# Kernel tuning notes

Measured on AMD Instinct MI355X. Metric: run time of the kernel, lower is better.

Reference implementation:

```python
import jax, jax.numpy as jnp
import numpy as np

TOP_K = 2
NUM_EXPERTS = 8


def setup_inputs() -> dict:
    key = jax.random.key(0)
    ks = jax.random.split(key, 9)
    B, S, N, H = 1, 8, 1024, 512
    E, I_moe, I_sh = NUM_EXPERTS, 2048 // TOP_K, 2048
    s = 0.02
    return {
        "hidden_states": jax.random.normal(ks[0], (B, S, N, H), dtype=jnp.float32),
        "gate_w": jax.random.normal(ks[1], (E, H), dtype=jnp.float32) * s,
        "expert_w1": jax.random.normal(ks[2], (E, I_moe, H), dtype=jnp.float32) * s,
        "expert_w2": jax.random.normal(ks[3], (E, H, I_moe), dtype=jnp.float32) * s,
        "expert_w3": jax.random.normal(ks[4], (E, I_moe, H), dtype=jnp.float32) * s,
        "shared_w1": jax.random.normal(ks[5], (I_sh, H), dtype=jnp.float32) * s,
        "shared_w2": jax.random.normal(ks[6], (H, I_sh), dtype=jnp.float32) * s,
        "shared_w3": jax.random.normal(ks[7], (I_sh, H), dtype=jnp.float32) * s,
        "shared_gate_w": jax.random.normal(ks[8], (1, H), dtype=jnp.float32) * s,
    }


def reference(hidden_states, gate_w, expert_w1, expert_w2, expert_w3,
              shared_w1, shared_w2, shared_w3, shared_gate_w):
    B, S, N, H = hidden_states.shape
    x = hidden_states.reshape(-1, H)                       # [T, H], T = B*S*N

    # Router: softmax in fp32, then top-k (norm_topk_prob=False).
    router_logits = x @ gate_w.T                           # [T, E]
    probs = jax.nn.softmax(router_logits.astype(jnp.float32), axis=-1)
    top_w, top_i = jax.lax.top_k(probs, TOP_K)             # [T, k]
    # Combine weight per (token, expert): zero for unselected experts.
    combine = jnp.sum(top_w[..., None] * jax.nn.one_hot(top_i, NUM_EXPERTS, dtype=probs.dtype), axis=1)
    combine = combine.astype(x.dtype)                      # [T, E]

    # Routed experts (SwiGLU FFN per expert), evaluated densely and masked
    # by the sparse combine weights (same math as gather/scatter dispatch).
    h1 = jnp.einsum('th,eih->tei', x, expert_w1)           # [T, E, I_moe]
    h3 = jnp.einsum('th,eih->tei', x, expert_w3)
    h = jax.nn.silu(h1) * h3
    expert_out = jnp.einsum('tei,ehi->teh', h, expert_w2)  # [T, E, H]
    moe_out = jnp.einsum('te,teh->th', combine, expert_out)

    # Shared expert with sigmoid gate.
    sh = (jax.nn.silu(x @ shared_w1.T) * (x @ shared_w3.T)) @ shared_w2.T
    sgate = jax.nn.sigmoid(x @ shared_gate_w.T)            # [T, 1]
    out = moe_out + sgate * sh

    return out.reshape(B, S, N, H), router_logits
```

## Files before the change

### kernel.cpp

```cpp
#include <hip/hip_runtime.h>
#include <hip/hip_bf16.h>
#include <stdint.h>
#include <math.h>

typedef __bf16 bf16;
typedef bf16 bf16x8 __attribute__((ext_vector_type(8)));
typedef bf16 bf16x4 __attribute__((ext_vector_type(4)));
typedef float f32x4 __attribute__((ext_vector_type(4)));
typedef unsigned int u32;

#define TOKENS 8192
#define HD 512
#define NE 8
#define IM 1024
#define ISH 2048
#define CAP 2560

__device__ __forceinline__ void gld16(const void* g, void* l) {
  __builtin_amdgcn_global_load_lds(
      (const __attribute__((address_space(1))) u32*)g,
      (__attribute__((address_space(3))) u32*)l, 16, 0, 0);
}

#define RT_BLOCKS (TOKENS / 4)
#define CVT_BLOCKS 3840
#define CVT_STRIDE (CVT_BLOCKS * 256)
#define F4_E  (NE * IM * HD / 4)
#define F4_S  (ISH * HD / 4)
#define F4_C1 (F4_E)
#define F4_C2 (F4_C1 + F4_E)
#define F4_C3 (F4_C2 + F4_S)
#define F4_C4 (F4_C3 + F4_S)
#define F4_C5 (F4_C4 + F4_E)
#define F4_TOT (F4_C5 + F4_S)

__launch_bounds__(256)
__global__ void router_cvt_k(const float* __restrict__ x, const float* __restrict__ gw,
                             const float* __restrict__ sgw, float* __restrict__ logits,
                             float* __restrict__ sgate, int* __restrict__ topi,
                             float* __restrict__ topw, int* __restrict__ counts,
                             bf16* __restrict__ xb,
                             const float* __restrict__ e1, const float* __restrict__ e3,
                             const float* __restrict__ s1, const float* __restrict__ s3,
                             const float* __restrict__ e2, const float* __restrict__ s2,
                             bf16* __restrict__ wdst) {
  if (blockIdx.x >= RT_BLOCKS) {
    int idx = (blockIdx.x - RT_BLOCKS) * 256 + threadIdx.x;
#pragma unroll
    for (int it = 0; it < 4; it++, idx += CVT_STRIDE) {
      const float* s; int off;
      if (idx < F4_C1)      { s = e1; off = idx; }
      else if (idx < F4_C2) { s = e3; off = idx - F4_C1; }
      else if (idx < F4_C3) { s = s1; off = idx - F4_C2; }
      else if (idx < F4_C4) { s = s3; off = idx - F4_C3; }
      else if (idx < F4_C5) { s = e2; off = idx - F4_C4; }
      else                  { s = s2; off = idx - F4_C5; }
      const float4 v = ((const float4*)s)[off];
      bf16x4 o;
      o.x = (bf16)v.x; o.y = (bf16)v.y; o.z = (bf16)v.z; o.w = (bf16)v.w;
      ((bf16x4*)wdst)[idx] = o;
    }
    return;
  }
  if (blockIdx.x == 0 && threadIdx.x < NE) counts[threadIdx.x] = 0;
  __shared__ float gws[9][512];
  for (int i = threadIdx.x; i < 9 * 512; i += 256) {
    int r = i >> 9, c = i & 511;
    float v = (r < 8) ? gw[i] : sgw[c];
    gws[r][((c & 7) << 6) | (c >> 3)] = v;
  }
  __syncthreads();
  int wave = threadIdx.x >> 6, lane = threadIdx.x & 63;
  int t = blockIdx.x * 4 + wave;
  const float* xp = x + (size_t)t * HD + lane * 8;
  float4 va = *(const float4*)xp;
  float4 vb = *(const float4*)(xp + 4);
  float xv[8] = {va.x, va.y, va.z, va.w, vb.x, vb.y, vb.z, vb.w};
  {
    bf16x8 xo;
#pragma unroll
    for (int j = 0; j < 8; j++) xo[j] = (bf16)xv[j];
    *(bf16x8*)(xb + (size_t)t * HD + lane * 8) = xo;
  }
  float acc[9];
#pragma unroll
  for (int e = 0; e < 9; e++) {
    float a = 0.f;
#pragma unroll
    for (int j = 0; j < 8; j++) a = fmaf(xv[j], gws[e][j * 64 + lane], a);
    acc[e] = a;
  }
#pragma unroll
  for (int off = 32; off > 0; off >>= 1) {
#pragma unroll
    for (int e = 0; e < 9; e++) acc[e] += __shfl_down(acc[e], off);
  }
  if (lane == 0) {
    float mx = acc[0];
#pragma unroll
    for (int e = 1; e < 8; e++) mx = fmaxf(mx, acc[e]);
    float p[8], sum = 0.f;
#pragma unroll
    for (int e = 0; e < 8; e++) { p[e] = expf(acc[e] - mx); sum += p[e]; }
    float inv = 1.f / sum;
    int i0 = 0; float b0 = p[0];
#pragma unroll
    for (int e = 1; e < 8; e++) if (p[e] > b0) { b0 = p[e]; i0 = e; }
    int i1 = -1; float b1 = -1.f;
#pragma unroll
    for (int e = 0; e < 8; e++) if (e != i0 && p[e] > b1) { b1 = p[e]; i1 = e; }
#pragma unroll
    for (int e = 0; e < 8; e++) logits[(size_t)t * 8 + e] = acc[e];
    topi[2 * t] = i0; topi[2 * t + 1] = i1;
    topw[2 * t] = b0 * inv; topw[2 * t + 1] = b1 * inv;
    sgate[t] = 1.f / (1.f + expf(-acc[8]));
  }
}

__launch_bounds__(256)
__global__ void dispatch_k(const int* __restrict__ topi, const float* __restrict__ topw,
                           int* __restrict__ counts, int* __restrict__ tok,
                           float* __restrict__ wl, int* __restrict__ pos) {
  __shared__ int lcnt[NE];
  __shared__ int lbase[NE];
  int tid = threadIdx.x;
  if (tid < NE) lcnt[tid] = 0;
  __syncthreads();
  int t = blockIdx.x * 256 + tid;
  int e0 = topi[2 * t], e1 = topi[2 * t + 1];
  float w0 = topw[2 * t], w1 = topw[2 * t + 1];
  int r0 = atomicAdd(&lcnt[e0], 1);
  int r1 = atomicAdd(&lcnt[e1], 1);
  __syncthreads();
  if (tid < NE) lbase[tid] = atomicAdd(&counts[tid], lcnt[tid]);
  __syncthreads();
  int p0 = lbase[e0] + r0;
  int p1 = lbase[e1] + r1;
  if (p0 < CAP) { tok[e0 * CAP + p0] = t; wl[e0 * CAP + p0] = w0; }
  if (p1 < CAP) { tok[e1 * CAP + p1] = t; wl[e1 * CAP + p1] = w1; }
  pos[2 * t]     = (p0 < CAP) ? e0 * CAP + p0 : -1;
  pos[2 * t + 1] = (p1 < CAP) ? e1 * CAP + p1 : -1;
}

__launch_bounds__(256, 4)
__global__ void gemm1_k(const bf16* __restrict__ X, const int* __restrict__ tokl,
                        const int* __restrict__ counts,
                        const bf16* __restrict__ e1w, const bf16* __restrict__ e3w,
                        const bf16* __restrict__ s1w, const bf16* __restrict__ s3w,
                        bf16* __restrict__ hmoe, bf16* __restrict__ hsh) {
  const bf16 *W1, *W3;
  bf16* Hout;
  const int* tl = nullptr;
  int cnt = 0, m0, n0, N;
  bool gather;
  int y = blockIdx.y;
  if (y < 160) {
    int e = y / 20, mt = y % 20;
    cnt = min(counts[e], CAP);
    if (mt * 128 >= cnt) return;
    gather = true;
    tl = tokl + e * CAP;
    W1 = e1w + (size_t)e * IM * HD;
    W3 = e3w + (size_t)e * IM * HD;
    Hout = hmoe + (size_t)e * CAP * IM;
    N = IM; m0 = mt * 128; n0 = blockIdx.x * 64;
  } else {
    int s = y - 160;
    gather = false;
    W1 = s1w; W3 = s3w; Hout = hsh; N = ISH;
    m0 = (s >> 1) * 128;
    n0 = ((s & 1) * 16 + blockIdx.x) * 64;
  }

  __shared__ __align__(16) bf16 As[2][128 * 32];
  __shared__ __align__(16) bf16 B1s[2][64 * 32];
  __shared__ __align__(16) bf16 B3s[2][64 * 32];

  int tid = threadIdx.x;
  int sr = tid >> 2;
  int colb = (tid & 3) * 16;
  int ar0, ar1;
  if (gather) {
    ar0 = tl[min(m0 + sr, cnt - 1)];
    ar1 = tl[min(m0 + 64 + sr, cnt - 1)];
  } else { ar0 = m0 + sr; ar1 = m0 + 64 + sr; }
  const char* apa = (const char*)(X + (size_t)ar0 * HD) + colb;
  const char* apb = (const char*)(X + (size_t)ar1 * HD) + colb;
  const char* bp1 = (const char*)(W1 + (size_t)(n0 + sr) * HD) + colb;
  const char* bp3 = (const char*)(W3 + (size_t)(n0 + sr) * HD) + colb;
  char* lA0a = (char*)&As[0][0] + tid * 16;
  char* lA0b = (char*)&As[1][0] + tid * 16;
  char* lA1a = (char*)&As[0][0] + 4096 + tid * 16;
  char* lA1b = (char*)&As[1][0] + 4096 + tid * 16;
  char* lB1a = (char*)&B1s[0][0] + tid * 16;
  char* lB1b = (char*)&B1s[1][0] + tid * 16;
  char* lB3a = (char*)&B3s[0][0] + tid * 16;
  char* lB3b = (char*)&B3s[1][0] + tid * 16;

  int wid = tid >> 6, lane = tid & 63;
  int wm = (wid >> 1) * 64, wn = (wid & 1) * 32;
  int lrow = lane & 15, lq = lane >> 4;

  f32x4 acc1[4][2] = {};
  f32x4 acc3[4][2] = {};

  for (int kb = 0; kb < 1024; kb += 128) {
    __syncthreads();
    gld16(apa + kb, lA0a);      gld16(apa + kb + 64, lA0b);
    gld16(apb + kb, lA1a);      gld16(apb + kb + 64, lA1b);
    gld16(bp1 + kb, lB1a);      gld16(bp1 + kb + 64, lB1b);
    gld16(bp3 + kb, lB3a);      gld16(bp3 + kb + 64, lB3b);
    __syncthreads();
#pragma unroll
    for (int ks = 0; ks < 2; ks++) {
      bf16x8 a[4], b1[2], b3[2];
#pragma unroll
      for (int i = 0; i < 4; i++)
        a[i] = *(const bf16x8*)&As[ks][(wm + i * 16 + lrow) * 32 + lq * 8];
#pragma unroll
      for (int j = 0; j < 2; j++) {
        b1[j] = *(const bf16x8*)&B1s[ks][(wn + j * 16 + lrow) * 32 + lq * 8];
        b3[j] = *(const bf16x8*)&B3s[ks][(wn + j * 16 + lrow) * 32 + lq * 8];
      }
#pragma unroll
      for (int i = 0; i < 4; i++)
#pragma unroll
        for (int j = 0; j < 2; j++) {
          acc1[i][j] = __builtin_amdgcn_mfma_f32_16x16x32_bf16(a[i], b1[j], acc1[i][j], 0, 0, 0);
          acc3[i][j] = __builtin_amdgcn_mfma_f32_16x16x32_bf16(a[i], b3[j], acc3[i][j], 0, 0, 0);
        }
    }
  }

#pragma unroll
  for (int i = 0; i < 4; i++)
#pragma unroll
    for (int r = 0; r < 4; r++) {
      int row = m0 + wm + i * 16 + lq * 4 + r;
#pragma unroll
      for (int j = 0; j < 2; j++) {
        float v1 = acc1[i][j][r], v3 = acc3[i][j][r];
        float hv = v1 / (1.f + __expf(-v1)) * v3;
        Hout[(size_t)row * N + (n0 + wn + j * 16 + lrow)] = (bf16)hv;
      }
    }
}

__launch_bounds__(256, 4)
__global__ void gemm2_k(const bf16* __restrict__ hmoe, const bf16* __restrict__ hsh,
                        const bf16* __restrict__ e2w, const bf16* __restrict__ s2w,
                        const float* __restrict__ wll, const int* __restrict__ counts,
                        bf16* __restrict__ yslot, bf16* __restrict__ ysh) {
  const bf16 *Hin, *W2;
  const float* wlp = nullptr;
  bf16* Yout;
  int cnt = 0, m0, K;
  bool weighted;
  int y = blockIdx.y;
  if (y < 64) {
    weighted = false;
    Hin = hsh; W2 = s2w; Yout = ysh; K = ISH; m0 = y * 128;
  } else {
    int e = (y - 64) / 20, mt = (y - 64) % 20;
    cnt = min(counts[e], CAP);
    if (mt * 128 >= cnt) return;
    weighted = true;
    Hin = hmoe + (size_t)e * CAP * IM;
    W2 = e2w + (size_t)e * HD * IM;
    wlp = wll + e * CAP;
    Yout = yslot + (size_t)e * CAP * HD;
    K = IM; m0 = mt * 128;
  }
  int n0 = blockIdx.x * 128;

  __shared__ __align__(16) bf16 As[2][128 * 32];
  __shared__ __align__(16) bf16 Bs[2][128 * 32];

  int tid = threadIdx.x;
  int sr = tid >> 2;
  int colb = (tid & 3) * 16;
  const char* apa = (const char*)(Hin + (size_t)(m0 + sr) * K) + colb;
  const char* apb = (const char*)(Hin + (size_t)(m0 + 64 + sr) * K) + colb;
  const char* bpa = (const char*)(W2 + (size_t)(n0 + sr) * K) + colb;
  const char* bpb = (const char*)(W2 + (size_t)(n0 + 64 + sr) * K) + colb;
  char* lA0a = (char*)&As[0][0] + tid * 16;
  char* lA0b = (char*)&As[1][0] + tid * 16;
  char* lA1a = (char*)&As[0][0] + 4096 + tid * 16;
  char* lA1b = (char*)&As[1][0] + 4096 + tid * 16;
  char* lB0a = (char*)&Bs[0][0] + tid * 16;
  char* lB0b = (char*)&Bs[1][0] + tid * 16;
  char* lB1a = (char*)&Bs[0][0] + 4096 + tid * 16;
  char* lB1b = (char*)&Bs[1][0] + 4096 + tid * 16;

  int wid = tid >> 6, lane = tid & 63;
  int wm = (wid >> 1) * 64, wn = (wid & 1) * 64;
  int lrow = lane & 15, lq = lane >> 4;

  f32x4 acc[4][4] = {};

  for (int kb = 0; kb < K * 2; kb += 128) {
    __syncthreads();
    gld16(apa + kb, lA0a);      gld16(apa + kb + 64, lA0b);
    gld16(apb + kb, lA1a);      gld16(apb + kb + 64, lA1b);
    gld16(bpa + kb, lB0a);      gld16(bpa + kb + 64, lB0b);
    gld16(bpb + kb, lB1a);      gld16(bpb + kb + 64, lB1b);
    __syncthreads();
#pragma unroll
    for (int ks = 0; ks < 2; ks++) {
      bf16x8 a[4], b[4];
#pragma unroll
      for (int i = 0; i < 4; i++) {
        a[i] = *(const bf16x8*)&As[ks][(wm + i * 16 + lrow) * 32 + lq * 8];
        b[i] = *(const bf16x8*)&Bs[ks][(wn + i * 16 + lrow) * 32 + lq * 8];
      }
#pragma unroll
      for (int i = 0; i < 4; i++)
#pragma unroll
        for (int j = 0; j < 4; j++)
          acc[i][j] = __builtin_amdgcn_mfma_f32_16x16x32_bf16(a[i], b[j], acc[i][j], 0, 0, 0);
    }
  }

#pragma unroll
  for (int i = 0; i < 4; i++)
#pragma unroll
    for (int r = 0; r < 4; r++) {
      int row = m0 + wm + i * 16 + lq * 4 + r;
      float w = weighted ? ((row < cnt) ? wlp[row] : 0.f) : 1.f;
      bf16* op = Yout + (size_t)row * HD;
#pragma unroll
      for (int j = 0; j < 4; j++)
        op[n0 + wn + j * 16 + lrow] = (bf16)(w * acc[i][j][r]);
    }
}

__launch_bounds__(256)
__global__ void combine_k(const bf16* __restrict__ yslot, const bf16* __restrict__ ysh,
                          const int* __restrict__ pos, const float* __restrict__ sgate,
                          float* __restrict__ out) {
  int wave = threadIdx.x >> 6, lane = threadIdx.x & 63;
  int t = blockIdx.x * 4 + wave;
  int p0 = pos[2 * t], p1 = pos[2 * t + 1];
  float g = sgate[t];
  int col = lane * 8;
  float acc[8];
  {
    const bf16x8 s = *(const bf16x8*)(ysh + (size_t)t * HD + col);
#pragma unroll
    for (int i = 0; i < 8; i++) acc[i] = g * (float)s[i];
  }
  if (p0 >= 0) {
    const bf16x8 v = *(const bf16x8*)(yslot + (size_t)p0 * HD + col);
#pragma unroll
    for (int i = 0; i < 8; i++) acc[i] += (float)v[i];
  }
  if (p1 >= 0) {
    const bf16x8 v = *(const bf16x8*)(yslot + (size_t)p1 * HD + col);
#pragma unroll
    for (int i = 0; i < 8; i++) acc[i] += (float)v[i];
  }
  float* op = out + (size_t)t * HD + col;
#pragma unroll
  for (int i = 0; i < 8; i++) op[i] = acc[i];
}

extern "C" void kernel_launch(void* const* d_in, const int* in_sizes, int n_in,
                              void* d_out, int out_size, void* d_ws, size_t ws_size,
                              hipStream_t stream) {
  const float* x   = (const float*)d_in[0];
  const float* gw  = (const float*)d_in[1];
  const float* ew1 = (const float*)d_in[2];
  const float* ew2 = (const float*)d_in[3];
  const float* ew3 = (const float*)d_in[4];
  const float* sw1 = (const float*)d_in[5];
  const float* sw2 = (const float*)d_in[6];
  const float* sw3 = (const float*)d_in[7];
  const float* sgw = (const float*)d_in[8];
  float* out = (float*)d_out;
  float* logits = out + (size_t)TOKENS * HD;

  char* w = (char*)d_ws;
  bf16* xb  = (bf16*)w; w += (size_t)TOKENS * HD * 2;
  bf16* e1b = (bf16*)w; w += (size_t)NE * IM * HD * 2;
  bf16* e3b = (bf16*)w; w += (size_t)NE * IM * HD * 2;
  bf16* s1b = (bf16*)w; w += (size_t)ISH * HD * 2;
  bf16* s3b = (bf16*)w; w += (size_t)ISH * HD * 2;
  bf16* e2b = (bf16*)w; w += (size_t)NE * HD * IM * 2;
  bf16* s2b = (bf16*)w; w += (size_t)HD * ISH * 2;
  float* sgate = (float*)w; w += TOKENS * 4;
  int*   topi  = (int*)w;   w += TOKENS * 2 * 4;
  float* topw  = (float*)w; w += TOKENS * 2 * 4;
  int*   counts = (int*)w;  w += 256;
  int*   tok   = (int*)w;   w += NE * CAP * 4;
  float* wl    = (float*)w; w += NE * CAP * 4;
  int*   pos   = (int*)w;   w += TOKENS * 2 * 4;
  bf16* hmoe = (bf16*)w; w += (size_t)NE * CAP * IM * 2;
  bf16* hsh  = (bf16*)w; w += (size_t)TOKENS * ISH * 2;
  bf16* yslot = xb;
  bf16* ysh   = (bf16*)((char*)xb + (size_t)NE * CAP * HD * 2);

  hipLaunchKernelGGL(router_cvt_k, dim3(RT_BLOCKS + CVT_BLOCKS), dim3(256), 0, stream,
                     x, gw, sgw, logits, sgate, topi, topw, counts, xb,
                     ew1, ew3, sw1, sw3, ew2, sw2, e1b);
  hipLaunchKernelGGL(dispatch_k, dim3(TOKENS / 256), dim3(256), 0, stream,
                     topi, topw, counts, tok, wl, pos);
  hipLaunchKernelGGL(gemm1_k, dim3(16, 160 + 128), dim3(256), 0, stream,
                     xb, tok, counts, e1b, e3b, s1b, s3b, hmoe, hsh);
  hipLaunchKernelGGL(gemm2_k, dim3(4, 64 + 160), dim3(256), 0, stream,
                     hmoe, hsh, e2b, s2b, wl, counts, yslot, ysh);
  hipLaunchKernelGGL(combine_k, dim3(TOKENS / 4), dim3(256), 0, stream,
                     yslot, ysh, pos, sgate, out);
}
```

Measured before the change: 270.2 us.

## Remap GEMM block indices across XCDs and split shared-expert GEMM2 over K

Both GEMM kernels now turn the linear block id into a remapped tile index (b&7)*stride + (b>>3). The intent is that consecutive tiles, which share weights and rows, land on the same XCD and reuse its L2. GEMM2 also splits the shared expert's K=2048 reduction into two halves written to separate partial buffers, which raises block count and shortens the long shared tiles. combine_k adds the two partial buffers before applying the gate. The split path needs extra workspace and falls back when there is not enough; it adds one more bf16 buffer pass and a second rounding step.

```diff
diff --git a/kernel.cpp b/kernel.cpp
--- a/kernel.cpp
+++ b/kernel.cpp
@@ -153,9 +153,10 @@
   const int* tl = nullptr;
   int cnt = 0, m0, n0, N;
   bool gather;
-  int y = blockIdx.y;
-  if (y < 160) {
-    int e = y / 20, mt = y % 20;
+  int b = blockIdx.y * 16 + blockIdx.x;
+  int L = (b & 7) * 576 + (b >> 3);
+  if (L < 2560) {
+    int e = L / 320, r = L % 320, mt = r >> 4;
     cnt = min(counts[e], CAP);
     if (mt * 128 >= cnt) return;
     gather = true;
@@ -163,13 +164,13 @@
     W1 = e1w + (size_t)e * IM * HD;
     W3 = e3w + (size_t)e * IM * HD;
     Hout = hmoe + (size_t)e * CAP * IM;
-    N = IM; m0 = mt * 128; n0 = blockIdx.x * 64;
+    N = IM; m0 = mt * 128; n0 = (r & 15) * 64;
   } else {
-    int s = y - 160;
+    int Ls = L - 2560;
     gather = false;
     W1 = s1w; W3 = s3w; Hout = hsh; N = ISH;
-    m0 = (s >> 1) * 128;
-    n0 = ((s & 1) * 16 + blockIdx.x) * 64;
+    m0 = (Ls >> 5) * 128;
+    n0 = (Ls & 31) * 64;
   }
 
   __shared__ __align__(16) bf16 As[2][128 * 32];
@@ -250,28 +251,53 @@
 __global__ void gemm2_k(const bf16* __restrict__ hmoe, const bf16* __restrict__ hsh,
                         const bf16* __restrict__ e2w, const bf16* __restrict__ s2w,
                         const float* __restrict__ wll, const int* __restrict__ counts,
-                        bf16* __restrict__ yslot, bf16* __restrict__ ysh) {
+                        bf16* __restrict__ yslot, bf16* __restrict__ ysh0,
+                        bf16* __restrict__ ysh1, int split) {
   const bf16 *Hin, *W2;
   const float* wlp = nullptr;
   bf16* Yout;
-  int cnt = 0, m0, K;
+  int cnt = 0, m0, n0, lda, Kb;
   bool weighted;
-  int y = blockIdx.y;
-  if (y < 64) {
-    weighted = false;
-    Hin = hsh; W2 = s2w; Yout = ysh; K = ISH; m0 = y * 128;
+  if (split) {
+    int b = blockIdx.y * 4 + blockIdx.x;
+    int L = (b & 7) * 144 + (b >> 3);
+    if (L < 512) {
+      weighted = false;
+      int m = L >> 3, half = (L >> 2) & 1, n = L & 3;
+      Hin = hsh + half * 1024;
+      W2  = s2w + half * 1024;
+      Yout = half ? ysh1 : ysh0;
+      lda = ISH; Kb = 1024; m0 = m * 128; n0 = n * 128;
+    } else {
+      int Lr = L - 512;
+      int e = Lr / 80, r = Lr % 80, mt = r >> 2;
+      cnt = min(counts[e], CAP);
+      if (mt * 128 >= cnt) return;
+      weighted = true;
+      Hin = hmoe + (size_t)e * CAP * IM;
+      W2 = e2w + (size_t)e * HD * IM;
+      wlp = wll + e * CAP;
+      Yout = yslot + (size_t)e * CAP * HD;
+      lda = IM; Kb = IM; m0 = mt * 128; n0 = (r & 3) * 128;
+    }
   } else {
-    int e = (y - 64) / 20, mt = (y - 64) % 20;
-    cnt = min(counts[e], CAP);
-    if (mt * 128 >= cnt) return;
-    weighted = true;
-    Hin = hmoe + (size_t)e * CAP * IM;
-    W2 = e2w + (size_t)e * HD * IM;
-    wlp = wll + e * CAP;
-    Yout = yslot + (size_t)e * CAP * HD;
-    K = IM; m0 = mt * 128;
-  }
-  int n0 = blockIdx.x * 128;
+    int y = blockIdx.y;
+    if (y < 64) {
+      weighted = false;
+      Hin = hsh; W2 = s2w; Yout = ysh0; lda = ISH; Kb = ISH; m0 = y * 128;
+    } else {
+      int e = (y - 64) / 20, mt = (y - 64) % 20;
+      cnt = min(counts[e], CAP);
+      if (mt * 128 >= cnt) return;
+      weighted = true;
+      Hin = hmoe + (size_t)e * CAP * IM;
+      W2 = e2w + (size_t)e * HD * IM;
+      wlp = wll + e * CAP;
+      Yout = yslot + (size_t)e * CAP * HD;
+      lda = IM; Kb = IM; m0 = mt * 128;
+    }
+    n0 = blockIdx.x * 128;
+  }
 
   __shared__ __align__(16) bf16 As[2][128 * 32];
   __shared__ __align__(16) bf16 Bs[2][128 * 32];
@@ -279,10 +305,10 @@
   int tid = threadIdx.x;
   int sr = tid >> 2;
   int colb = (tid & 3) * 16;
-  const char* apa = (const char*)(Hin + (size_t)(m0 + sr) * K) + colb;
-  const char* apb = (const char*)(Hin + (size_t)(m0 + 64 + sr) * K) + colb;
-  const char* bpa = (const char*)(W2 + (size_t)(n0 + sr) * K) + colb;
-  const char* bpb = (const char*)(W2 + (size_t)(n0 + 64 + sr) * K) + colb;
+  const char* apa = (const char*)(Hin + (size_t)(m0 + sr) * lda) + colb;
+  const char* apb = (const char*)(Hin + (size_t)(m0 + 64 + sr) * lda) + colb;
+  const char* bpa = (const char*)(W2 + (size_t)(n0 + sr) * lda) + colb;
+  const char* bpb = (const char*)(W2 + (size_t)(n0 + 64 + sr) * lda) + colb;
   char* lA0a = (char*)&As[0][0] + tid * 16;
   char* lA0b = (char*)&As[1][0] + tid * 16;
   char* lA1a = (char*)&As[0][0] + 4096 + tid * 16;
@@ -298,7 +324,7 @@
 
   f32x4 acc[4][4] = {};
 
-  for (int kb = 0; kb < K * 2; kb += 128) {
+  for (int kb = 0; kb < Kb * 2; kb += 128) {
     __syncthreads();
     gld16(apa + kb, lA0a);      gld16(apa + kb + 64, lA0b);
     gld16(apb + kb, lA1a);      gld16(apb + kb + 64, lA1b);
@@ -307,17 +333,17 @@
     __syncthreads();
 #pragma unroll
     for (int ks = 0; ks < 2; ks++) {
-      bf16x8 a[4], b[4];
+      bf16x8 a[4], bb[4];
 #pragma unroll
       for (int i = 0; i < 4; i++) {
         a[i] = *(const bf16x8*)&As[ks][(wm + i * 16 + lrow) * 32 + lq * 8];
-        b[i] = *(const bf16x8*)&Bs[ks][(wn + i * 16 + lrow) * 32 + lq * 8];
+        bb[i] = *(const bf16x8*)&Bs[ks][(wn + i * 16 + lrow) * 32 + lq * 8];
       }
 #pragma unroll
       for (int i = 0; i < 4; i++)
 #pragma unroll
         for (int j = 0; j < 4; j++)
-          acc[i][j] = __builtin_amdgcn_mfma_f32_16x16x32_bf16(a[i], b[j], acc[i][j], 0, 0, 0);
+          acc[i][j] = __builtin_amdgcn_mfma_f32_16x16x32_bf16(a[i], bb[j], acc[i][j], 0, 0, 0);
     }
   }
 
@@ -335,9 +361,10 @@
 }
 
 __launch_bounds__(256)
-__global__ void combine_k(const bf16* __restrict__ yslot, const bf16* __restrict__ ysh,
-                          const int* __restrict__ pos, const float* __restrict__ sgate,
-                          float* __restrict__ out) {
+__global__ void combine_k(const bf16* __restrict__ yslot, const bf16* __restrict__ ysh0,
+                          const bf16* __restrict__ ysh1, const int* __restrict__ pos,
+                          const float* __restrict__ sgate, float* __restrict__ out,
+                          int split) {
   int wave = threadIdx.x >> 6, lane = threadIdx.x & 63;
   int t = blockIdx.x * 4 + wave;
   int p0 = pos[2 * t], p1 = pos[2 * t + 1];
@@ -345,9 +372,16 @@
   int col = lane * 8;
   float acc[8];
   {
-    const bf16x8 s = *(const bf16x8*)(ysh + (size_t)t * HD + col);
-#pragma unroll
-    for (int i = 0; i < 8; i++) acc[i] = g * (float)s[i];
+    const bf16x8 s0 = *(const bf16x8*)(ysh0 + (size_t)t * HD + col);
+#pragma unroll
+    for (int i = 0; i < 8; i++) acc[i] = (float)s0[i];
+    if (split) {
+      const bf16x8 s1 = *(const bf16x8*)(ysh1 + (size_t)t * HD + col);
+#pragma unroll
+      for (int i = 0; i < 8; i++) acc[i] += (float)s1[i];
+    }
+#pragma unroll
+    for (int i = 0; i < 8; i++) acc[i] *= g;
   }
   if (p0 >= 0) {
     const bf16x8 v = *(const bf16x8*)(yslot + (size_t)p0 * HD + col);
@@ -397,17 +431,20 @@
   bf16* hmoe = (bf16*)w; w += (size_t)NE * CAP * IM * 2;
   bf16* hsh  = (bf16*)w; w += (size_t)TOKENS * ISH * 2;
   bf16* yslot = xb;
-  bf16* ysh   = (bf16*)((char*)xb + (size_t)NE * CAP * HD * 2);
+  bf16* ysh0  = (bf16*)((char*)xb + (size_t)NE * CAP * HD * 2);
+  size_t need = (size_t)((char*)w - (char*)d_ws) + (size_t)TOKENS * HD * 2;
+  int split = (ws_size >= need) ? 1 : 0;
+  bf16* ysh1 = split ? (bf16*)w : ysh0;
 
   hipLaunchKernelGGL(router_cvt_k, dim3(RT_BLOCKS + CVT_BLOCKS), dim3(256), 0, stream,
                      x, gw, sgw, logits, sgate, topi, topw, counts, xb,
                      ew1, ew3, sw1, sw3, ew2, sw2, e1b);
   hipLaunchKernelGGL(dispatch_k, dim3(TOKENS / 256), dim3(256), 0, stream,
                      topi, topw, counts, tok, wl, pos);
-  hipLaunchKernelGGL(gemm1_k, dim3(16, 160 + 128), dim3(256), 0, stream,
+  hipLaunchKernelGGL(gemm1_k, dim3(16, 288), dim3(256), 0, stream,
                      xb, tok, counts, e1b, e3b, s1b, s3b, hmoe, hsh);
-  hipLaunchKernelGGL(gemm2_k, dim3(4, 64 + 160), dim3(256), 0, stream,
-                     hmoe, hsh, e2b, s2b, wl, counts, yslot, ysh);
+  hipLaunchKernelGGL(gemm2_k, dim3(4, split ? 288 : 224), dim3(256), 0, stream,
+                     hmoe, hsh, e2b, s2b, wl, counts, yslot, ysh0, ysh1, split);
   hipLaunchKernelGGL(combine_k, dim3(TOKENS / 4), dim3(256), 0, stream,
-                     yslot, ysh, pos, sgate, out);
-}
+                     yslot, ysh0, ysh1, pos, sgate, out, split);
+}
```

Measured after the change: 276.8 us. 2.4% more time.
